# Kernel tuning notes

Measured on AMD Instinct MI355X. Metric: run time of the kernel, lower is better.

Reference implementation:

```python
import jax, jax.numpy as jnp
import numpy as np

NEG_INF = -1.0e12  # matches masked_fill value in the torch module


def _entmax15(x, axis=-1):
    """Exact entmax with alpha=1.5 (Peters & Martins, 2019), sort-based."""
    x = x - jnp.max(x, axis=axis, keepdims=True)
    x = x / 2.0
    d = x.shape[axis]
    xs = -jnp.sort(-x, axis=axis)  # descending sort along normalization axis
    rho = jnp.arange(1, d + 1, dtype=x.dtype)  # 1..d, broadcasts on last axis
    mean = jnp.cumsum(xs, axis=axis) / rho
    mean_sq = jnp.cumsum(xs * xs, axis=axis) / rho
    ss = rho * (mean_sq - mean * mean)
    delta = (1.0 - ss) / rho
    tau = mean - jnp.sqrt(jnp.clip(delta, 0.0))
    support = jnp.sum((tau <= xs).astype(jnp.int32), axis=axis, keepdims=True)
    tau_star = jnp.take_along_axis(tau, support - 1, axis=axis)
    y = jnp.clip(x - tau_star, 0.0)
    return y * y


def setup_inputs() -> dict:
    key = jax.random.key(0)
    kq, kk, kv, km = jax.random.split(key, 4)
    B, H, S, D = 4, 8, 1024, 128
    q = jax.random.normal(kq, (B, H, S, D), dtype=jnp.float32)
    k = jax.random.normal(kk, (B, H, S, D), dtype=jnp.float32)
    v = jax.random.normal(kv, (B, H, S, D), dtype=jnp.float32)
    mask = jax.random.randint(km, (B, 1, S, S), 0, 2, dtype=jnp.int32)
    return {"q": q, "k": k, "v": v, "mask": mask}


def reference(q, k, v, mask):
    D = q.shape[-1]
    scale = 1.0 / jnp.sqrt(jnp.asarray(D, dtype=q.dtype))
    scores = jnp.einsum("bhqd,bhkd->bhqk", q, k) * scale
    scores = jnp.where(mask == 0, jnp.asarray(NEG_INF, dtype=scores.dtype), scores)
    attn = _entmax15(scores, axis=-1)
    return jnp.einsum("bhqk,bhkd->bhqd", attn, v)
```

## Files before the change

kernel.cpp:

```cpp
#include <hip/hip_runtime.h>


#define S_ 1024
#define D_ 128
#define NEG_INF_F (-1.0e12f)
#define SCALE_F 0.08838834764831845f
#define NITER 14

typedef float f32x4 __attribute__((ext_vector_type(4)));
typedef short short8 __attribute__((ext_vector_type(8)));

__device__ __forceinline__ ushort f2bf(float x) {
    unsigned u = __builtin_bit_cast(unsigned, x);
    u += 0x7FFFu + ((u >> 16) & 1u);
    return (ushort)(u >> 16);
}
__device__ __forceinline__ float bf2f(ushort h) {
    unsigned u = ((unsigned)h) << 16;
    return __builtin_bit_cast(float, u);
}

__global__ __launch_bounds__(256)
void pre_cvt(const float* __restrict__ K, const float* __restrict__ V,
             ushort* __restrict__ Kb, ushort* __restrict__ Vt)
{
    __shared__ __align__(16) ushort tileT[64][68];
    const int t = threadIdx.x;
    if (blockIdx.x < 4096) {
        int i = blockIdx.x * 256 + t;
        float4 v = ((const float4*)K)[i];
        ushort4 o;
        o.x = f2bf(v.x); o.y = f2bf(v.y); o.z = f2bf(v.z); o.w = f2bf(v.w);
        ((ushort4*)Kb)[i] = o;
        return;
    }
    const int vb = blockIdx.x - 4096;
    const int bh = vb >> 5, r5 = vb & 31, kt = r5 >> 1, dh = r5 & 1;
    const float* src = V + ((size_t)(bh * S_ + kt * 64)) * D_ + dh * 64;
    #pragma unroll
    for (int i = 0; i < 4; ++i) {
        int idx = t + i * 256, r = idx >> 4, c = idx & 15;
        float4 vv = *(const float4*)(src + (size_t)r * D_ + c * 4);
        tileT[c * 4 + 0][r] = f2bf(vv.x);
        tileT[c * 4 + 1][r] = f2bf(vv.y);
        tileT[c * 4 + 2][r] = f2bf(vv.z);
        tileT[c * 4 + 3][r] = f2bf(vv.w);
    }
    __syncthreads();
    ushort* dst = Vt + ((size_t)(bh * D_ + dh * 64)) * S_ + kt * 64;
    #pragma unroll
    for (int i = 0; i < 2; ++i) {
        int idx = t + i * 256, d = idx >> 3, jj = idx & 7;
        short8 val = *(const short8*)&tileT[d][jj * 8];
        *(short8*)(dst + (size_t)d * S_ + jj * 8) = val;
    }
}

__global__ __launch_bounds__(512, 8)
void entmax_attn(const float* __restrict__ Q, const ushort* __restrict__ Kb,
                 const ushort* __restrict__ Vt, const int* __restrict__ M,
                 float* __restrict__ O)
{
    __shared__ __align__(16) ushort sc[16][1024];
    __shared__ __align__(16) ushort q_s[16][128];

    const int t = threadIdx.x;
    const int w = t >> 6, lane = t & 63, l = lane & 15, quad = lane >> 4;
    const int bh = blockIdx.x >> 6, qt = blockIdx.x & 63, b = bh >> 3;

    const ushort* kb_bh = Kb + (size_t)bh * (S_ * D_);
    const ushort* vt_bh = Vt + (size_t)bh * (D_ * S_);

    {
        const float4* qsrc = (const float4*)(Q + ((size_t)bh * S_ + (size_t)qt * 16) * D_);
        int r = t >> 5, c = t & 31;
        float4 v = qsrc[r * 32 + c];
        ushort4 o;
        o.x = f2bf(v.x); o.y = f2bf(v.y); o.z = f2bf(v.z); o.w = f2bf(v.w);
        *(ushort4*)&q_s[r][(((c >> 1) ^ (r & 7)) << 3) + ((c & 1) << 2)] = o;
    }

    const ushort* kp = kb_bh + (size_t)(w * 16 + l) * D_ + quad * 8;
    short8 c0 = *(const short8*)(kp +  0);
    short8 c1 = *(const short8*)(kp + 32);
    short8 c2 = *(const short8*)(kp + 64);
    short8 c3 = *(const short8*)(kp + 96);

    __syncthreads();

    short8 aq[4];
    #pragma unroll
    for (int ks = 0; ks < 4; ++ks)
        aq[ks] = *(const short8*)&q_s[l][((ks * 4 + quad) ^ (l & 7)) << 3];

    #pragma unroll 1
    for (int kt = 0; kt < 7; ++kt) {
        const ushort* np = kp + (size_t)(kt + 1) * (128 * D_);
        short8 n0 = *(const short8*)(np +  0);
        short8 n1 = *(const short8*)(np + 32);
        short8 n2 = *(const short8*)(np + 64);
        short8 n3 = *(const short8*)(np + 96);
        f32x4 acc = {0.f, 0.f, 0.f, 0.f};
        __builtin_amdgcn_s_setprio(1);
        acc = __builtin_amdgcn_mfma_f32_16x16x32_bf16(aq[0], c0, acc, 0, 0, 0);
        acc = __builtin_amdgcn_mfma_f32_16x16x32_bf16(aq[1], c1, acc, 0, 0, 0);
        acc = __builtin_amdgcn_mfma_f32_16x16x32_bf16(aq[2], c2, acc, 0, 0, 0);
        acc = __builtin_amdgcn_mfma_f32_16x16x32_bf16(aq[3], c3, acc, 0, 0, 0);
        __builtin_amdgcn_s_setprio(0);
        const int coln = kt * 16 + w * 2 + (l >> 3);
        #pragma unroll
        for (int r = 0; r < 4; ++r) {
            const int rr = quad * 4 + r;
            sc[rr][((coln ^ (rr & 7)) << 3) + (l & 7)] = f2bf(acc[r] * SCALE_F);
        }
        c0 = n0; c1 = n1; c2 = n2; c3 = n3;
    }
    {
        f32x4 acc = {0.f, 0.f, 0.f, 0.f};
        __builtin_amdgcn_s_setprio(1);
        acc = __builtin_amdgcn_mfma_f32_16x16x32_bf16(aq[0], c0, acc, 0, 0, 0);
        acc = __builtin_amdgcn_mfma_f32_16x16x32_bf16(aq[1], c1, acc, 0, 0, 0);
        acc = __builtin_amdgcn_mfma_f32_16x16x32_bf16(aq[2], c2, acc, 0, 0, 0);
        acc = __builtin_amdgcn_mfma_f32_16x16x32_bf16(aq[3], c3, acc, 0, 0, 0);
        __builtin_amdgcn_s_setprio(0);
        const int coln = 7 * 16 + w * 2 + (l >> 3);
        #pragma unroll
        for (int r = 0; r < 4; ++r) {
            const int rr = quad * 4 + r;
            sc[rr][((coln ^ (rr & 7)) << 3) + (l & 7)] = f2bf(acc[r] * SCALE_F);
        }
    }
    __syncthreads();

    const int row = t >> 5, u = t & 31;
    const int qg = qt * 16 + row;
    float x[32];
    #pragma unroll
    for (int c = 0; c < 4; ++c) {
        short8 v8 = *(const short8*)&sc[row][((c * 32 + u) ^ (row & 7)) << 3];
        #pragma unroll
        for (int e = 0; e < 8; ++e) x[c * 8 + e] = bf2f(((ushort*)&v8)[e]);
    }
    {
        const int4* mrow = (const int4*)(M + ((size_t)b * S_ + qg) * S_);
        #pragma unroll
        for (int c = 0; c < 4; ++c) {
            #pragma unroll
            for (int h = 0; h < 2; ++h) {
                int4 mm = mrow[c * 64 + u * 2 + h];
                if (mm.x == 0) x[c * 8 + h * 4 + 0] = NEG_INF_F;
                if (mm.y == 0) x[c * 8 + h * 4 + 1] = NEG_INF_F;
                if (mm.z == 0) x[c * 8 + h * 4 + 2] = NEG_INF_F;
                if (mm.w == 0) x[c * 8 + h * 4 + 3] = NEG_INF_F;
            }
        }
    }
    float mx = -3.0e38f;
    #pragma unroll
    for (int j = 0; j < 32; ++j) mx = fmaxf(mx, x[j]);
    #pragma unroll
    for (int off = 1; off < 32; off <<= 1) mx = fmaxf(mx, __shfl_xor(mx, off));
    #pragma unroll
    for (int j = 0; j < 32; ++j) x[j] = (x[j] - mx) * 0.5f;

    float lo = -1.f, hi = 0.f;
    #pragma unroll 1
    for (int it = 0; it < NITER; ++it) {
        const float tm = 0.5f * (lo + hi);
        float f = 0.f;
        #pragma unroll
        for (int j = 0; j < 32; ++j) {
            float d = fmaxf(x[j] - tm, 0.f);
            f = fmaf(d, d, f);
        }
        #pragma unroll
        for (int off = 1; off < 32; off <<= 1) f += __shfl_xor(f, off);
        const bool ge = (f >= 1.f);
        lo = ge ? tm : lo;
        hi = ge ? hi : tm;
    }
    const float tau = 0.5f * (lo + hi);

    #pragma unroll
    for (int c = 0; c < 4; ++c) {
        short8 v8;
        #pragma unroll
        for (int e = 0; e < 8; ++e) {
            float d = fmaxf(x[c * 8 + e] - tau, 0.f);
            ((ushort*)&v8)[e] = f2bf(d * d);
        }
        *(short8*)&sc[row][((c * 32 + u) ^ (row & 7)) << 3] = v8;
    }

    const ushort* vp = vt_bh + (size_t)(w * 16 + l) * S_ + quad * 8;
    c0 = *(const short8*)(vp +  0);
    c1 = *(const short8*)(vp + 32);
    c2 = *(const short8*)(vp + 64);
    c3 = *(const short8*)(vp + 96);
    __syncthreads();

    f32x4 oa = {0.f, 0.f, 0.f, 0.f};
    #pragma unroll 1
    for (int vt = 0; vt < 7; ++vt) {
        const ushort* np = vp + (size_t)(vt + 1) * 128;
        short8 n0 = *(const short8*)(np +  0);
        short8 n1 = *(const short8*)(np + 32);
        short8 n2 = *(const short8*)(np + 64);
        short8 n3 = *(const short8*)(np + 96);
        short8 a0 = *(const short8*)&sc[l][((vt * 16 +  0 + quad) ^ (l & 7)) << 3];
        short8 a1 = *(const short8*)&sc[l][((vt * 16 +  4 + quad) ^ (l & 7)) << 3];
        short8 a2 = *(const short8*)&sc[l][((vt * 16 +  8 + quad) ^ (l & 7)) << 3];
        short8 a3 = *(const short8*)&sc[l][((vt * 16 + 12 + quad) ^ (l & 7)) << 3];
        __builtin_amdgcn_s_setprio(1);
        oa = __builtin_amdgcn_mfma_f32_16x16x32_bf16(a0, c0, oa, 0, 0, 0);
        oa = __builtin_amdgcn_mfma_f32_16x16x32_bf16(a1, c1, oa, 0, 0, 0);
        oa = __builtin_amdgcn_mfma_f32_16x16x32_bf16(a2, c2, oa, 0, 0, 0);
        oa = __builtin_amdgcn_mfma_f32_16x16x32_bf16(a3, c3, oa, 0, 0, 0);
        __builtin_amdgcn_s_setprio(0);
        c0 = n0; c1 = n1; c2 = n2; c3 = n3;
    }
    {
        short8 a0 = *(const short8*)&sc[l][((7 * 16 +  0 + quad) ^ (l & 7)) << 3];
        short8 a1 = *(const short8*)&sc[l][((7 * 16 +  4 + quad) ^ (l & 7)) << 3];
        short8 a2 = *(const short8*)&sc[l][((7 * 16 +  8 + quad) ^ (l & 7)) << 3];
        short8 a3 = *(const short8*)&sc[l][((7 * 16 + 12 + quad) ^ (l & 7)) << 3];
        __builtin_amdgcn_s_setprio(1);
        oa = __builtin_amdgcn_mfma_f32_16x16x32_bf16(a0, c0, oa, 0, 0, 0);
        oa = __builtin_amdgcn_mfma_f32_16x16x32_bf16(a1, c1, oa, 0, 0, 0);
        oa = __builtin_amdgcn_mfma_f32_16x16x32_bf16(a2, c2, oa, 0, 0, 0);
        oa = __builtin_amdgcn_mfma_f32_16x16x32_bf16(a3, c3, oa, 0, 0, 0);
        __builtin_amdgcn_s_setprio(0);
    }

    float* ob = O + ((size_t)bh * S_ + (size_t)qt * 16) * D_;
    #pragma unroll
    for (int r = 0; r < 4; ++r)
        ob[(size_t)(quad * 4 + r) * D_ + w * 16 + l] = oa[r];
}

extern "C" void kernel_launch(void* const* d_in, const int* in_sizes, int n_in,
                              void* d_out, int out_size, void* d_ws, size_t ws_size,
                              hipStream_t stream) {
    const float* q = (const float*)d_in[0];
    const float* k = (const float*)d_in[1];
    const float* v = (const float*)d_in[2];
    const int*   m = (const int*)d_in[3];
    float*       o = (float*)d_out;

    ushort* Kb = (ushort*)d_ws;
    ushort* Vt = (ushort*)((char*)d_ws + 8388608);

    pre_cvt<<<5120, 256, 0, stream>>>(k, v, Kb, Vt);
    entmax_attn<<<2048, 512, 0, stream>>>(q, Kb, Vt, m, o);
}
```

Baseline: 226.9 us.

## Load Q fragments directly to registers, swizzle block order, relax launch bounds

Q rows are now loaded straight from global memory into MFMA A-fragments and converted to bf16 in registers, which removes the shared-memory Q staging buffer and one block barrier. Block indices are remapped so that consecutive blocks are spread across bh groups, likely to improve L2 locality for K/V across XCDs. The launch-bounds occupancy hint drops from 8 to 3 so the compiler has more registers available. Each lane now issues uncoalesced 32-byte Q loads per row, and the lower occupancy hint may reduce latency hiding.

```diff
diff --git a/kernel.cpp b/kernel.cpp
--- a/kernel.cpp
+++ b/kernel.cpp
@@ -18,6 +18,12 @@
 __device__ __forceinline__ float bf2f(ushort h) {
     unsigned u = ((unsigned)h) << 16;
     return __builtin_bit_cast(float, u);
+}
+__device__ __forceinline__ short8 cvt8(float4 a, float4 b) {
+    short8 r; ushort* p = (ushort*)&r;
+    p[0] = f2bf(a.x); p[1] = f2bf(a.y); p[2] = f2bf(a.z); p[3] = f2bf(a.w);
+    p[4] = f2bf(b.x); p[5] = f2bf(b.y); p[6] = f2bf(b.z); p[7] = f2bf(b.w);
+    return r;
 }
 
 __global__ __launch_bounds__(256)
@@ -56,28 +62,30 @@
     }
 }
 
-__global__ __launch_bounds__(512, 8)
+__global__ __launch_bounds__(512, 3)
 void entmax_attn(const float* __restrict__ Q, const ushort* __restrict__ Kb,
                  const ushort* __restrict__ Vt, const int* __restrict__ M,
                  float* __restrict__ O)
 {
     __shared__ __align__(16) ushort sc[16][1024];
-    __shared__ __align__(16) ushort q_s[16][128];
 
     const int t = threadIdx.x;
     const int w = t >> 6, lane = t & 63, l = lane & 15, quad = lane >> 4;
-    const int bh = blockIdx.x >> 6, qt = blockIdx.x & 63, b = bh >> 3;
+    const int swz = (blockIdx.x & 7) * 256 + (blockIdx.x >> 3);
+    const int bh = swz >> 6, qt = swz & 63, b = bh >> 3;
 
     const ushort* kb_bh = Kb + (size_t)bh * (S_ * D_);
     const ushort* vt_bh = Vt + (size_t)bh * (D_ * S_);
 
-    {
-        const float4* qsrc = (const float4*)(Q + ((size_t)bh * S_ + (size_t)qt * 16) * D_);
-        int r = t >> 5, c = t & 31;
-        float4 v = qsrc[r * 32 + c];
-        ushort4 o;
-        o.x = f2bf(v.x); o.y = f2bf(v.y); o.z = f2bf(v.z); o.w = f2bf(v.w);
-        *(ushort4*)&q_s[r][(((c >> 1) ^ (r & 7)) << 3) + ((c & 1) << 2)] = o;
+    short8 aq[4];
+    {
+        const float* qr = Q + ((size_t)(bh * S_ + qt * 16 + l)) * D_ + quad * 8;
+        #pragma unroll
+        for (int ks = 0; ks < 4; ++ks) {
+            float4 qa = *(const float4*)(qr + ks * 32);
+            float4 qb = *(const float4*)(qr + ks * 32 + 4);
+            aq[ks] = cvt8(qa, qb);
+        }
     }
 
     const ushort* kp = kb_bh + (size_t)(w * 16 + l) * D_ + quad * 8;
@@ -85,13 +93,6 @@
     short8 c1 = *(const short8*)(kp + 32);
     short8 c2 = *(const short8*)(kp + 64);
     short8 c3 = *(const short8*)(kp + 96);
-
-    __syncthreads();
-
-    short8 aq[4];
-    #pragma unroll
-    for (int ks = 0; ks < 4; ++ks)
-        aq[ks] = *(const short8*)&q_s[l][((ks * 4 + quad) ^ (l & 7)) << 3];
 
     #pragma unroll 1
     for (int kt = 0; kt < 7; ++kt) {
@@ -193,10 +194,10 @@
     }
 
     const ushort* vp = vt_bh + (size_t)(w * 16 + l) * S_ + quad * 8;
-    c0 = *(const short8*)(vp +  0);
-    c1 = *(const short8*)(vp + 32);
-    c2 = *(const short8*)(vp + 64);
-    c3 = *(const short8*)(vp + 96);
+    short8 v0 = *(const short8*)(vp +  0);
+    short8 v1 = *(const short8*)(vp + 32);
+    short8 v2 = *(const short8*)(vp + 64);
+    short8 v3 = *(const short8*)(vp + 96);
     __syncthreads();
 
     f32x4 oa = {0.f, 0.f, 0.f, 0.f};
@@ -212,12 +213,12 @@
         short8 a2 = *(const short8*)&sc[l][((vt * 16 +  8 + quad) ^ (l & 7)) << 3];
         short8 a3 = *(const short8*)&sc[l][((vt * 16 + 12 + quad) ^ (l & 7)) << 3];
         __builtin_amdgcn_s_setprio(1);
-        oa = __builtin_amdgcn_mfma_f32_16x16x32_bf16(a0, c0, oa, 0, 0, 0);
-        oa = __builtin_amdgcn_mfma_f32_16x16x32_bf16(a1, c1, oa, 0, 0, 0);
-        oa = __builtin_amdgcn_mfma_f32_16x16x32_bf16(a2, c2, oa, 0, 0, 0);
-        oa = __builtin_amdgcn_mfma_f32_16x16x32_bf16(a3, c3, oa, 0, 0, 0);
-        __builtin_amdgcn_s_setprio(0);
-        c0 = n0; c1 = n1; c2 = n2; c3 = n3;
+        oa = __builtin_amdgcn_mfma_f32_16x16x32_bf16(a0, v0, oa, 0, 0, 0);
+        oa = __builtin_amdgcn_mfma_f32_16x16x32_bf16(a1, v1, oa, 0, 0, 0);
+        oa = __builtin_amdgcn_mfma_f32_16x16x32_bf16(a2, v2, oa, 0, 0, 0);
+        oa = __builtin_amdgcn_mfma_f32_16x16x32_bf16(a3, v3, oa, 0, 0, 0);
+        __builtin_amdgcn_s_setprio(0);
+        v0 = n0; v1 = n1; v2 = n2; v3 = n3;
     }
     {
         short8 a0 = *(const short8*)&sc[l][((7 * 16 +  0 + quad) ^ (l & 7)) << 3];
@@ -225,10 +226,10 @@
         short8 a2 = *(const short8*)&sc[l][((7 * 16 +  8 + quad) ^ (l & 7)) << 3];
         short8 a3 = *(const short8*)&sc[l][((7 * 16 + 12 + quad) ^ (l & 7)) << 3];
         __builtin_amdgcn_s_setprio(1);
-        oa = __builtin_amdgcn_mfma_f32_16x16x32_bf16(a0, c0, oa, 0, 0, 0);
-        oa = __builtin_amdgcn_mfma_f32_16x16x32_bf16(a1, c1, oa, 0, 0, 0);
-        oa = __builtin_amdgcn_mfma_f32_16x16x32_bf16(a2, c2, oa, 0, 0, 0);
-        oa = __builtin_amdgcn_mfma_f32_16x16x32_bf16(a3, c3, oa, 0, 0, 0);
+        oa = __builtin_amdgcn_mfma_f32_16x16x32_bf16(a0, v0, oa, 0, 0, 0);
+        oa = __builtin_amdgcn_mfma_f32_16x16x32_bf16(a1, v1, oa, 0, 0, 0);
+        oa = __builtin_amdgcn_mfma_f32_16x16x32_bf16(a2, v2, oa, 0, 0, 0);
+        oa = __builtin_amdgcn_mfma_f32_16x16x32_bf16(a3, v3, oa, 0, 0, 0);
         __builtin_amdgcn_s_setprio(0);
     }
 
```

After: 234.9 us. +3.5%, slower.
